# Performance work log

Measured on AMD Instinct MI355X. Metric: run time of the kernel, lower is better.

Reference implementation:

```python
import jax, jax.numpy as jnp
import numpy as np

B, S, D_IN, D, H, HD, HALF, L = 64, 500, 64, 128, 8, 16, 5, 2
WIN = 2 * HALF + 1  # 11 attended positions per query
EPS = 1e-12  # HF layer_norm_eps default


def _ln(x, g, b):
    m = x.mean(-1, keepdims=True)
    v = ((x - m) ** 2).mean(-1, keepdims=True)
    return (x - m) / jnp.sqrt(v + EPS) * g + b


def setup_inputs() -> dict:
    key = jax.random.key(0)
    ks = jax.random.split(key, 24)
    n = lambda i, shape: jax.random.normal(ks[i], shape, jnp.float32) * 0.02
    return {
        "x": jax.random.normal(ks[0], (B, S, D_IN), jnp.float32),
        "W_in": n(1, (D_IN, D)), "b_in": jnp.zeros((D,), jnp.float32),
        "pos_emb": n(2, (512, D)), "tt_emb": n(3, (D,)),
        "ln_emb_g": jnp.ones((D,), jnp.float32), "ln_emb_b": jnp.zeros((D,), jnp.float32),
        "Wq": n(4, (L, D, D)), "bq": jnp.zeros((L, D), jnp.float32),
        "Wk": n(5, (L, D, D)), "bk": jnp.zeros((L, D), jnp.float32),
        "Wv": n(6, (L, D, D)), "bv": jnp.zeros((L, D), jnp.float32),
        "Wo": n(7, (L, D, D)), "bo": jnp.zeros((L, D), jnp.float32),
        "ln1_g": jnp.ones((L, D), jnp.float32), "ln1_b": jnp.zeros((L, D), jnp.float32),
        "Wi": n(8, (L, D, 512)), "bi": jnp.zeros((L, 512), jnp.float32),
        "Wo2": n(9, (L, 512, D)), "bo2": jnp.zeros((L, D), jnp.float32),
        "ln2_g": jnp.ones((L, D), jnp.float32), "ln2_b": jnp.zeros((L, D), jnp.float32),
        "W_cls": n(10, (D, 2)), "b_cls": jnp.zeros((2,), jnp.float32),
    }


def reference(x, W_in, b_in, pos_emb, tt_emb, ln_emb_g, ln_emb_b,
              Wq, bq, Wk, bk, Wv, bv, Wo, bo, ln1_g, ln1_b,
              Wi, bi, Wo2, bo2, ln2_g, ln2_b, W_cls, b_cls):
    # input projection + RoBERTa-style embeddings (position ids start at padding_idx+1=2)
    h = x @ W_in + b_in
    pos_ids = 2 + jnp.arange(S)
    h = _ln(h + pos_emb[pos_ids] + tt_emb, ln_emb_g, ln_emb_b)

    # sliding-window gather indices: each query attends [i-HALF, i+HALF]
    idx = jnp.arange(S)[:, None] + jnp.arange(-HALF, HALF + 1)[None, :]
    valid = (idx >= 0) & (idx < S)
    idxc = jnp.clip(idx, 0, S - 1)
    scale = 1.0 / jnp.sqrt(jnp.float32(HD))

    for l in range(L):
        qh = (h @ Wq[l] + bq[l]).reshape(B, S, H, HD).transpose(0, 2, 1, 3)
        kh = (h @ Wk[l] + bk[l]).reshape(B, S, H, HD).transpose(0, 2, 1, 3)
        vh = (h @ Wv[l] + bv[l]).reshape(B, S, H, HD).transpose(0, 2, 1, 3)
        kk = kh[:, :, idxc]
        scores = jnp.einsum('bhsd,bhswd->bhsw', qh * scale, kk)
        scores = jnp.where(valid, scores, -jnp.inf)
        probs = jax.nn.softmax(scores, axis=-1)
        vv = vh[:, :, idxc]
        ctx = jnp.einsum('bhsw,bhswd->bhsd', probs, vv)
        ctx = ctx.transpose(0, 2, 1, 3).reshape(B, S, D)
        h = _ln(ctx @ Wo[l] + bo[l] + h, ln1_g[l], ln1_b[l])
        ff = jax.nn.gelu(h @ Wi[l] + bi[l], approximate=False) @ Wo2[l] + bo2[l]
        h = _ln(ff + h, ln2_g[l], ln2_b[l])

    pooled = h.mean(axis=1)  # mean over sequence
    return pooled @ W_cls + b_cls
```

## Files before the change

kernel.cpp:

```cpp
#include <hip/hip_runtime.h>
#include <hip/hip_bf16.h>
#include <math.h>

#define BB 64
#define SS 500
#define DIN 64
#define DD 128
#define HH 8
#define HDIM 16
#define HALF_ 5
#define WINW 11
#define LL 2
#define FF 512
#define MM (BB*SS)
#define LN_EPS 1e-12f

typedef __attribute__((ext_vector_type(8))) short short8;
typedef __attribute__((ext_vector_type(4))) float f32x4;

__global__ __launch_bounds__(256) void k_prep(
    const float* __restrict__ Wq, const float* __restrict__ Wk,
    const float* __restrict__ Wv, const float* __restrict__ Wo,
    const float* __restrict__ Wi, const float* __restrict__ Wo2,
    const float* __restrict__ Win, __hip_bfloat16* __restrict__ wT)
{
    const int m = blockIdx.y;
    const float* src; int Kd, Nd, kshift, doff;
    if (m == 12) {
        src = Win; Kd = 64; Nd = 128; kshift = 6; doff = 393216;
    } else {
        const int l = m / 6, t = m % 6;
        int toff;
        switch (t) {
          case 0:  src = Wq  + l*16384; Kd=128; Nd=128; kshift=7; toff=0;      break;
          case 1:  src = Wk  + l*16384; Kd=128; Nd=128; kshift=7; toff=16384;  break;
          case 2:  src = Wv  + l*16384; Kd=128; Nd=128; kshift=7; toff=32768;  break;
          case 3:  src = Wo  + l*16384; Kd=128; Nd=128; kshift=7; toff=49152;  break;
          case 4:  src = Wi  + l*65536; Kd=128; Nd=512; kshift=7; toff=65536;  break;
          default: src = Wo2 + l*65536; Kd=512; Nd=128; kshift=9; toff=131072; break;
        }
        doff = l*196608 + toff;
    }
    __hip_bfloat16* dst = wT + doff;
    const int NK = Kd * Nd;
    int e = (blockIdx.x * 256 + threadIdx.x) * 4;
    if (e >= NK) return;
    #pragma unroll
    for (int j = 0; j < 4; ++j, ++e) {
        int n = e >> kshift, kx = e & (Kd - 1);
        dst[(size_t)n * Kd + kx] = __float2bfloat16(src[(size_t)kx * Nd + n]);
    }
}

__global__ __launch_bounds__(256) void k_xcvt(
    const float* __restrict__ x, __hip_bfloat16* __restrict__ xbf)
{
    int i = (blockIdx.x * 256 + threadIdx.x) * 4;
    if (i >= MM * DIN) return;
    float4 v = *(const float4*)(x + i);
    ushort4 o;
    __hip_bfloat16 t0 = __float2bfloat16(v.x); o.x = *(unsigned short*)&t0;
    __hip_bfloat16 t1 = __float2bfloat16(v.y); o.y = *(unsigned short*)&t1;
    __hip_bfloat16 t2 = __float2bfloat16(v.z); o.z = *(unsigned short*)&t2;
    __hip_bfloat16 t3 = __float2bfloat16(v.w); o.w = *(unsigned short*)&t3;
    *(ushort4*)(xbf + i) = o;
}

#define GEMM_MAIN(Abf, lda, Kdim, WTbf, ldw, n0w)                             \
    __shared__ __align__(16) __hip_bfloat16 As[64][72];                       \
    __shared__ __align__(16) __hip_bfloat16 Ws[128][72];                      \
    const int tid = threadIdx.x;                                              \
    const int wid = tid >> 6;                                                 \
    const int l15 = tid & 15;                                                 \
    const int l4  = (tid & 63) >> 4;                                          \
    const int m0  = blockIdx.x * 64;                                          \
    f32x4 acc[8];                                                             \
    _Pragma("unroll")                                                         \
    for (int n = 0; n < 8; ++n) acc[n] = (f32x4){0.f, 0.f, 0.f, 0.f};         \
    for (int k0 = 0; k0 < (Kdim); k0 += 64) {                                 \
        _Pragma("unroll")                                                     \
        for (int it = 0; it < 2; ++it) {                                      \
            int lin = it * 2048 + tid * 8;                                    \
            int r = lin >> 6, c = lin & 63;                                   \
            *(uint4*)&As[r][c] =                                              \
                *(const uint4*)((Abf) + (size_t)(m0 + r) * (lda) + k0 + c);   \
        }                                                                     \
        _Pragma("unroll")                                                     \
        for (int it = 0; it < 4; ++it) {                                      \
            int lin = it * 2048 + tid * 8;                                    \
            int r = lin >> 6, c = lin & 63;                                   \
            *(uint4*)&Ws[r][c] =                                              \
                *(const uint4*)((WTbf) + (size_t)((n0w) + r) * (ldw) + k0 + c); \
        }                                                                     \
        __syncthreads();                                                      \
        _Pragma("unroll")                                                     \
        for (int kc = 0; kc < 64; kc += 32) {                                 \
            short8 a0 = *(const short8*)&As[wid * 16 + l15][kc + l4 * 8];     \
            _Pragma("unroll")                                                 \
            for (int n = 0; n < 8; ++n) {                                     \
                short8 bf = *(const short8*)&Ws[n * 16 + l15][kc + l4 * 8];   \
                acc[n] = __builtin_amdgcn_mfma_f32_16x16x32_bf16(a0, bf, acc[n], 0, 0, 0); \
            }                                                                 \
        }                                                                     \
        __syncthreads();                                                      \
    }

__global__ __launch_bounds__(256, 4) void k_embed(
    const __hip_bfloat16* __restrict__ xbf, const __hip_bfloat16* __restrict__ wInT,
    const float* __restrict__ bin, const float* __restrict__ pos,
    const float* __restrict__ tt, const float* __restrict__ g,
    const float* __restrict__ be, float* __restrict__ h,
    __hip_bfloat16* __restrict__ hbf)
{
    GEMM_MAIN(xbf, DIN, DIN, wInT, DIN, 0)
    #pragma unroll
    for (int qq = 0; qq < 4; ++qq) {
        const int row = m0 + wid * 16 + l4 * 4 + qq;
        const int s = row % SS;
        float vals[8]; float s1 = 0.f, s2 = 0.f;
        #pragma unroll
        for (int n = 0; n < 8; ++n) {
            const int col = n * 16 + l15;
            float val = acc[n][qq] + bin[col] + tt[col] + pos[(size_t)(2 + s) * DD + col];
            vals[n] = val; s1 += val; s2 += val * val;
        }
        #pragma unroll
        for (int o = 1; o < 16; o <<= 1) {
            s1 += __shfl_xor(s1, o, 16);
            s2 += __shfl_xor(s2, o, 16);
        }
        const float mean = s1 * (1.0f / DD);
        const float var  = s2 * (1.0f / DD) - mean * mean;
        const float rstd = rsqrtf(var + LN_EPS);
        #pragma unroll
        for (int n = 0; n < 8; ++n) {
            const int col = n * 16 + l15;
            const float o = (vals[n] - mean) * rstd * g[col] + be[col];
            h[(size_t)row * DD + col]   = o;
            hbf[(size_t)row * DD + col] = __float2bfloat16(o);
        }
    }
}

__global__ __launch_bounds__(512, 4) void k_fused(
    const __hip_bfloat16* __restrict__ hin,
    const __hip_bfloat16* __restrict__ wTq, const __hip_bfloat16* __restrict__ wTk,
    const __hip_bfloat16* __restrict__ wTv, const __hip_bfloat16* __restrict__ wTo,
    const float* __restrict__ bq, const float* __restrict__ bk,
    const float* __restrict__ bv, const float* __restrict__ bo,
    const float* __restrict__ hres,
    const float* __restrict__ g1, const float* __restrict__ bt1,
    float* __restrict__ hout, __hip_bfloat16* __restrict__ hbfout)
{
    __shared__ __align__(16) char smem[51072];
    __hip_bfloat16* kS   = (__hip_bfloat16*)smem;
    __hip_bfloat16* vS   = (__hip_bfloat16*)(smem + 13056);
    __hip_bfloat16* hS   = (__hip_bfloat16*)(smem + 26112);
    __hip_bfloat16* qS   = (__hip_bfloat16*)(smem + 39168);
    float*          pS   = (float*)(smem + 47872);
    float*          rsum = (float*)(smem + 50048);
    __hip_bfloat16* ctxS = hS;

    const int tid = threadIdx.x;
    const int wid = tid >> 6;
    const int l15 = tid & 15, l4 = (tid & 63) >> 4;
    const int b = blockIdx.y;
    const int s0 = blockIdx.x * 32;

    #pragma unroll
    for (int it = 0; it < 2; ++it) {
        int lin = it * 512 + tid;
        if (lin < 768) {
            int r = lin >> 4, c8 = (lin & 15) * 8;
            int s = s0 - 5 + r;
            uint4 val = {0, 0, 0, 0};
            if (s >= 0 && s < SS)
                val = *(const uint4*)(hin + ((size_t)(b * SS + s)) * DD + c8);
            *(uint4*)&hS[r * 136 + c8] = val;
        }
    }
    __syncthreads();

    #pragma unroll
    for (int i = 0; i < 9; ++i) {
        const int t = wid + i * 8;
        const int out = t / 24;
        const int rem = t - out * 24;
        const int rt = rem >> 3, n = rem & 7;
        const __hip_bfloat16* WT = (out == 0) ? wTq : ((out == 1) ? wTk : wTv);
        const float* bias = (out == 0) ? bq : ((out == 1) ? bk : bv);
        f32x4 a = (f32x4){0.f, 0.f, 0.f, 0.f};
        #pragma unroll
        for (int kc = 0; kc < 4; ++kc) {
            short8 af  = *(const short8*)&hS[(rt * 16 + l15) * 136 + kc * 32 + l4 * 8];
            short8 bfg = *(const short8*)(WT + (size_t)(n * 16 + l15) * DD + kc * 32 + l4 * 8);
            a = __builtin_amdgcn_mfma_f32_16x16x32_bf16(af, bfg, a, 0, 0, 0);
        }
        const int col = n * 16 + l15;
        const float bcol = bias[col];
        #pragma unroll
        for (int qq = 0; qq < 4; ++qq) {
            const int row = rt * 16 + l4 * 4 + qq;
            const float val = a[qq] + bcol;
            if (out == 0) {
                if (row >= 5 && row < 37)
                    qS[(row - 5) * 136 + col] = __float2bfloat16(val * 0.25f);
            } else if (out == 1) {
                kS[row * 136 + col] = __float2bfloat16(val);
            } else {
                vS[row * 136 + col] = __float2bfloat16(val);
            }
        }
    }
    __syncthreads();

    {
        const int g = tid >> 4, wl = tid & 15;
        const int sq = s0 + g;
        const int sk = sq + wl - HALF_;
        const bool valid = (wl < WINW) && (sq < SS) && (sk >= 0) && (sk < SS);
        #pragma unroll
        for (int hh = 0; hh < 8; ++hh) {
            const int off = hh * 16;
            float sc = 0.f;
            const unsigned* qp = (const unsigned*)&qS[g * 136 + off];
            const unsigned* kp = (const unsigned*)&kS[(g + wl) * 136 + off];
            #pragma unroll
            for (int d2 = 0; d2 < 8; ++d2) {
                unsigned qu = qp[d2], ku = kp[d2];
                sc += __uint_as_float(qu << 16) * __uint_as_float(ku << 16)
                    + __uint_as_float(qu & 0xffff0000u) * __uint_as_float(ku & 0xffff0000u);
            }
            sc = valid ? sc : -INFINITY;
            float mx = sc;
            #pragma unroll
            for (int o = 1; o < 16; o <<= 1) mx = fmaxf(mx, __shfl_xor(mx, o, 16));
            float p = valid ? __expf(sc - mx) : 0.f;
            float den = p;
            #pragma unroll
            for (int o = 1; o < 16; o <<= 1) den += __shfl_xor(den, o, 16);
            const float inv = (den > 0.f) ? 1.f / den : 0.f;
            pS[g * 17 + wl] = p;
            float cd = 0.f;
            #pragma unroll
            for (int w2 = 0; w2 < WINW; ++w2)
                cd += pS[g * 17 + w2] * __bfloat162float(vS[(g + w2) * 136 + off + wl]);
            ctxS[g * 136 + off + wl] = __float2bfloat16(cd * inv);
        }
    }
    __syncthreads();

    const int rt2 = wid & 1, nh = wid >> 1;
    f32x4 ac[2];
    #pragma unroll
    for (int n4 = 0; n4 < 2; ++n4) {
        ac[n4] = (f32x4){0.f, 0.f, 0.f, 0.f};
        const int n = nh * 2 + n4;
        #pragma unroll
        for (int kc = 0; kc < 4; ++kc) {
            short8 af  = *(const short8*)&ctxS[(rt2 * 16 + l15) * 136 + kc * 32 + l4 * 8];
            short8 bfg = *(const short8*)(wTo + (size_t)(n * 16 + l15) * DD + kc * 32 + l4 * 8);
            ac[n4] = __builtin_amdgcn_mfma_f32_16x16x32_bf16(af, bfg, ac[n4], 0, 0, 0);
        }
    }
    float vals[4][2];
    #pragma unroll
    for (int qq = 0; qq < 4; ++qq) {
        const int r16 = l4 * 4 + qq;
        const int qrow = rt2 * 16 + r16;
        const int sq = s0 + qrow;
        const bool vr = (sq < SS);
        float s1 = 0.f, s2 = 0.f;
        #pragma unroll
        for (int n4 = 0; n4 < 2; ++n4) {
            const int col = (nh * 2 + n4) * 16 + l15;
            const float resv = vr ? hres[((size_t)(b * SS + sq)) * DD + col] : 0.f;
            const float val = ac[n4][qq] + bo[col] + resv;
            vals[qq][n4] = val; s1 += val; s2 += val * val;
        }
        #pragma unroll
        for (int o = 1; o < 16; o <<= 1) {
            s1 += __shfl_xor(s1, o, 16);
            s2 += __shfl_xor(s2, o, 16);
        }
        if (l15 == 0) {
            rsum[((rt2 * 4 + nh) * 16 + r16) * 2]     = s1;
            rsum[((rt2 * 4 + nh) * 16 + r16) * 2 + 1] = s2;
        }
    }
    __syncthreads();
    #pragma unroll
    for (int qq = 0; qq < 4; ++qq) {
        const int r16 = l4 * 4 + qq;
        const int qrow = rt2 * 16 + r16;
        const int sq = s0 + qrow;
        if (sq >= SS) continue;
        float S1 = 0.f, S2 = 0.f;
        #pragma unroll
        for (int j = 0; j < 4; ++j) {
            S1 += rsum[((rt2 * 4 + j) * 16 + r16) * 2];
            S2 += rsum[((rt2 * 4 + j) * 16 + r16) * 2 + 1];
        }
        const float mean = S1 * (1.0f / DD);
        const float var  = S2 * (1.0f / DD) - mean * mean;
        const float rstd = rsqrtf(var + LN_EPS);
        #pragma unroll
        for (int n4 = 0; n4 < 2; ++n4) {
            const int col = (nh * 2 + n4) * 16 + l15;
            const float o = (vals[qq][n4] - mean) * rstd * g1[col] + bt1[col];
            hout[((size_t)(b * SS + sq)) * DD + col]   = o;
            hbfout[((size_t)(b * SS + sq)) * DD + col] = __float2bfloat16(o);
        }
    }
}

__global__ __launch_bounds__(256, 4) void k_gemm_gelu(
    const __hip_bfloat16* __restrict__ hbf,
    const __hip_bfloat16* __restrict__ wTi,
    const float* __restrict__ bias, __hip_bfloat16* __restrict__ hid)
{
    const int n0g = blockIdx.y * 128;
    GEMM_MAIN(hbf, DD, DD, wTi, DD, n0g)
    #pragma unroll
    for (int qq = 0; qq < 4; ++qq) {
        const int row = m0 + wid * 16 + l4 * 4 + qq;
        #pragma unroll
        for (int n = 0; n < 8; ++n) {
            const int col = n0g + n * 16 + l15;
            float val = acc[n][qq] + bias[col];
            val = 0.5f * val * (1.f + erff(val * 0.70710678118f));
            hid[(size_t)row * FF + col] = __float2bfloat16(val);
        }
    }
}

__global__ __launch_bounds__(256, 4) void k_gemm_lnres(
    const __hip_bfloat16* __restrict__ Abf, int lda, int Kdim,
    const __hip_bfloat16* __restrict__ WT,
    const float* __restrict__ bias, const float* __restrict__ res,
    const float* __restrict__ g, const float* __restrict__ bt,
    float* __restrict__ outF, __hip_bfloat16* __restrict__ outB)
{
    GEMM_MAIN(Abf, lda, Kdim, WT, Kdim, 0)
    #pragma unroll
    for (int qq = 0; qq < 4; ++qq) {
        const int row = m0 + wid * 16 + l4 * 4 + qq;
        float vals[8]; float s1 = 0.f, s2 = 0.f;
        #pragma unroll
        for (int n = 0; n < 8; ++n) {
            const int col = n * 16 + l15;
            float val = acc[n][qq] + bias[col] + res[(size_t)row * DD + col];
            vals[n] = val; s1 += val; s2 += val * val;
        }
        #pragma unroll
        for (int o = 1; o < 16; o <<= 1) {
            s1 += __shfl_xor(s1, o, 16);
            s2 += __shfl_xor(s2, o, 16);
        }
        const float mean = s1 * (1.0f / DD);
        const float var  = s2 * (1.0f / DD) - mean * mean;
        const float rstd = rsqrtf(var + LN_EPS);
        #pragma unroll
        for (int n = 0; n < 8; ++n) {
            const int col = n * 16 + l15;
            const float o = (vals[n] - mean) * rstd * g[col] + bt[col];
            outF[(size_t)row * DD + col] = o;
            outB[(size_t)row * DD + col] = __float2bfloat16(o);
        }
    }
}

__global__ __launch_bounds__(128) void k_final(
    const float* __restrict__ h, const float* __restrict__ Wc,
    const float* __restrict__ bc, float* __restrict__ out)
{
    const int b = blockIdx.x, d = threadIdx.x;
    float p = 0.f;
    for (int s = 0; s < SS; ++s) p += h[((size_t)(b * SS + s)) * DD + d];
    p *= (1.0f / SS);
    float l0 = p * Wc[d * 2 + 0];
    float l1 = p * Wc[d * 2 + 1];
    #pragma unroll
    for (int off = 1; off < 64; off <<= 1) {
        l0 += __shfl_xor(l0, off);
        l1 += __shfl_xor(l1, off);
    }
    __shared__ float r[2][2];
    const int wid = d >> 6;
    if ((d & 63) == 0) { r[wid][0] = l0; r[wid][1] = l1; }
    __syncthreads();
    if (d == 0) {
        out[b * 2 + 0] = r[0][0] + r[1][0] + bc[0];
        out[b * 2 + 1] = r[0][1] + r[1][1] + bc[1];
    }
}

extern "C" void kernel_launch(void* const* d_in, const int* in_sizes, int n_in,
                              void* d_out, int out_size, void* d_ws, size_t ws_size,
                              hipStream_t stream)
{
    const float* x      = (const float*)d_in[0];
    const float* W_in   = (const float*)d_in[1];
    const float* b_in   = (const float*)d_in[2];
    const float* pos    = (const float*)d_in[3];
    const float* tt     = (const float*)d_in[4];
    const float* lng    = (const float*)d_in[5];
    const float* lnb    = (const float*)d_in[6];
    const float* Wq     = (const float*)d_in[7];
    const float* bq     = (const float*)d_in[8];
    const float* Wk     = (const float*)d_in[9];
    const float* bk     = (const float*)d_in[10];
    const float* Wv     = (const float*)d_in[11];
    const float* bv     = (const float*)d_in[12];
    const float* Wo     = (const float*)d_in[13];
    const float* bo     = (const float*)d_in[14];
    const float* ln1g   = (const float*)d_in[15];
    const float* ln1b   = (const float*)d_in[16];
    const float* Wi     = (const float*)d_in[17];
    const float* bi     = (const float*)d_in[18];
    const float* Wo2    = (const float*)d_in[19];
    const float* bo2    = (const float*)d_in[20];
    const float* ln2g   = (const float*)d_in[21];
    const float* ln2b   = (const float*)d_in[22];
    const float* Wc     = (const float*)d_in[23];
    const float* bc     = (const float*)d_in[24];

    float*          ws   = (float*)d_ws;
    float*          hA   = ws;
    __hip_bfloat16* hbA  = (__hip_bfloat16*)(ws + 4096000);
    __hip_bfloat16* xbf  = (__hip_bfloat16*)(ws + 6144000);
    __hip_bfloat16* wT   = (__hip_bfloat16*)(ws + 7168000);
    __hip_bfloat16* hid  = (__hip_bfloat16*)(ws + 7368704);
    float*          hB   = ws + 15560704;
    __hip_bfloat16* hbB  = (__hip_bfloat16*)(ws + 19656704);

    k_prep<<<dim3(64, 13), 256, 0, stream>>>(Wq, Wk, Wv, Wo, Wi, Wo2, W_in, wT);
    k_xcvt<<<2000, 256, 0, stream>>>(x, xbf);
    k_embed<<<MM / 64, 256, 0, stream>>>(xbf, wT + 393216, b_in, pos, tt, lng, lnb,
                                         hA, hbA);

    float* hI = hA; __hip_bfloat16* hbI = hbA;
    float* hO = hB; __hip_bfloat16* hbO = hbB;
    for (int l = 0; l < LL; ++l) {
        const __hip_bfloat16* wTq  = wT + l * 196608;
        const __hip_bfloat16* wTk  = wTq + 16384;
        const __hip_bfloat16* wTv  = wTq + 32768;
        const __hip_bfloat16* wTo  = wTq + 49152;
        const __hip_bfloat16* wTi  = wTq + 65536;
        const __hip_bfloat16* wTo2 = wTq + 131072;

        k_fused<<<dim3(16, BB), 512, 0, stream>>>(
            hbI, wTq, wTk, wTv, wTo,
            bq + l * DD, bk + l * DD, bv + l * DD, bo + l * DD,
            hI, ln1g + l * DD, ln1b + l * DD, hO, hbO);

        k_gemm_gelu<<<dim3(MM / 64, 4), 256, 0, stream>>>(
            hbO, wTi, bi + l * FF, hid);

        k_gemm_lnres<<<dim3(MM / 64, 1), 256, 0, stream>>>(
            hid, FF, FF, wTo2, bo2 + l * DD, hO, ln2g + l * DD, ln2b + l * DD,
            hO, hbO);

        float* tf = hI; hI = hO; hO = tf;
        __hip_bfloat16* tb = hbI; hbI = hbO; hbO = tb;
    }

    k_final<<<BB, 128, 0, stream>>>(hI, Wc, bc, (float*)d_out);
}
```

Baseline: 336.8 us.

## Fuse FFN up-projection, GELU and down-projection into the attention kernel

Folds the FFN (Wi GEMM plus GELU, then the Wo2 GEMM with residual and LayerNorm) into the per-tile attention kernel. The post-LN1 activations and the 32x512 hidden tile stay in shared memory, reusing the K/V/h/q buffers. This removes two kernel launches per layer and the global write and read of the bf16 hidden tensor. In exchange, only 32 rows are processed per block, so FFN weight reuse is lower, and weights are read straight from global memory for every block.

```diff
diff --git a/kernel.cpp b/kernel.cpp
--- a/kernel.cpp
+++ b/kernel.cpp
@@ -146,10 +146,13 @@
     const __hip_bfloat16* __restrict__ hin,
     const __hip_bfloat16* __restrict__ wTq, const __hip_bfloat16* __restrict__ wTk,
     const __hip_bfloat16* __restrict__ wTv, const __hip_bfloat16* __restrict__ wTo,
+    const __hip_bfloat16* __restrict__ wTi, const __hip_bfloat16* __restrict__ wTo2,
     const float* __restrict__ bq, const float* __restrict__ bk,
     const float* __restrict__ bv, const float* __restrict__ bo,
+    const float* __restrict__ bi, const float* __restrict__ bo2,
     const float* __restrict__ hres,
     const float* __restrict__ g1, const float* __restrict__ bt1,
+    const float* __restrict__ g2, const float* __restrict__ bt2,
     float* __restrict__ hout, __hip_bfloat16* __restrict__ hbfout)
 {
     __shared__ __align__(16) char smem[51072];
@@ -160,6 +163,8 @@
     float*          pS   = (float*)(smem + 47872);
     float*          rsum = (float*)(smem + 50048);
     __hip_bfloat16* ctxS = hS;
+    __hip_bfloat16* h1S  = qS;
+    __hip_bfloat16* hidS = (__hip_bfloat16*)smem;
 
     const int tid = threadIdx.x;
     const int wid = tid >> 6;
@@ -251,121 +256,148 @@
     __syncthreads();
 
     const int rt2 = wid & 1, nh = wid >> 1;
-    f32x4 ac[2];
-    #pragma unroll
-    for (int n4 = 0; n4 < 2; ++n4) {
-        ac[n4] = (f32x4){0.f, 0.f, 0.f, 0.f};
-        const int n = nh * 2 + n4;
-        #pragma unroll
-        for (int kc = 0; kc < 4; ++kc) {
-            short8 af  = *(const short8*)&ctxS[(rt2 * 16 + l15) * 136 + kc * 32 + l4 * 8];
-            short8 bfg = *(const short8*)(wTo + (size_t)(n * 16 + l15) * DD + kc * 32 + l4 * 8);
-            ac[n4] = __builtin_amdgcn_mfma_f32_16x16x32_bf16(af, bfg, ac[n4], 0, 0, 0);
-        }
-    }
-    float vals[4][2];
-    #pragma unroll
-    for (int qq = 0; qq < 4; ++qq) {
-        const int r16 = l4 * 4 + qq;
-        const int qrow = rt2 * 16 + r16;
-        const int sq = s0 + qrow;
-        const bool vr = (sq < SS);
-        float s1 = 0.f, s2 = 0.f;
+    {
+        f32x4 ac[2];
         #pragma unroll
         for (int n4 = 0; n4 < 2; ++n4) {
-            const int col = (nh * 2 + n4) * 16 + l15;
-            const float resv = vr ? hres[((size_t)(b * SS + sq)) * DD + col] : 0.f;
-            const float val = ac[n4][qq] + bo[col] + resv;
-            vals[qq][n4] = val; s1 += val; s2 += val * val;
-        }
-        #pragma unroll
-        for (int o = 1; o < 16; o <<= 1) {
-            s1 += __shfl_xor(s1, o, 16);
-            s2 += __shfl_xor(s2, o, 16);
-        }
-        if (l15 == 0) {
-            rsum[((rt2 * 4 + nh) * 16 + r16) * 2]     = s1;
-            rsum[((rt2 * 4 + nh) * 16 + r16) * 2 + 1] = s2;
-        }
-    }
-    __syncthreads();
-    #pragma unroll
-    for (int qq = 0; qq < 4; ++qq) {
-        const int r16 = l4 * 4 + qq;
-        const int qrow = rt2 * 16 + r16;
-        const int sq = s0 + qrow;
-        if (sq >= SS) continue;
-        float S1 = 0.f, S2 = 0.f;
-        #pragma unroll
-        for (int j = 0; j < 4; ++j) {
-            S1 += rsum[((rt2 * 4 + j) * 16 + r16) * 2];
-            S2 += rsum[((rt2 * 4 + j) * 16 + r16) * 2 + 1];
-        }
-        const float mean = S1 * (1.0f / DD);
-        const float var  = S2 * (1.0f / DD) - mean * mean;
-        const float rstd = rsqrtf(var + LN_EPS);
+            ac[n4] = (f32x4){0.f, 0.f, 0.f, 0.f};
+            const int n = nh * 2 + n4;
+            #pragma unroll
+            for (int kc = 0; kc < 4; ++kc) {
+                short8 af  = *(const short8*)&ctxS[(rt2 * 16 + l15) * 136 + kc * 32 + l4 * 8];
+                short8 bfg = *(const short8*)(wTo + (size_t)(n * 16 + l15) * DD + kc * 32 + l4 * 8);
+                ac[n4] = __builtin_amdgcn_mfma_f32_16x16x32_bf16(af, bfg, ac[n4], 0, 0, 0);
+            }
+        }
+        float vals[4][2];
+        #pragma unroll
+        for (int qq = 0; qq < 4; ++qq) {
+            const int r16 = l4 * 4 + qq;
+            const int qrow = rt2 * 16 + r16;
+            const int sq = s0 + qrow;
+            const bool vr = (sq < SS);
+            float s1 = 0.f, s2 = 0.f;
+            #pragma unroll
+            for (int n4 = 0; n4 < 2; ++n4) {
+                const int col = (nh * 2 + n4) * 16 + l15;
+                const float resv = vr ? hres[((size_t)(b * SS + sq)) * DD + col] : 0.f;
+                const float val = ac[n4][qq] + bo[col] + resv;
+                vals[qq][n4] = val; s1 += val; s2 += val * val;
+            }
+            #pragma unroll
+            for (int o = 1; o < 16; o <<= 1) {
+                s1 += __shfl_xor(s1, o, 16);
+                s2 += __shfl_xor(s2, o, 16);
+            }
+            if (l15 == 0) {
+                rsum[((rt2 * 4 + nh) * 16 + r16) * 2]     = s1;
+                rsum[((rt2 * 4 + nh) * 16 + r16) * 2 + 1] = s2;
+            }
+        }
+        __syncthreads();
+        #pragma unroll
+        for (int qq = 0; qq < 4; ++qq) {
+            const int r16 = l4 * 4 + qq;
+            const int qrow = rt2 * 16 + r16;
+            float S1 = 0.f, S2 = 0.f;
+            #pragma unroll
+            for (int j = 0; j < 4; ++j) {
+                S1 += rsum[((rt2 * 4 + j) * 16 + r16) * 2];
+                S2 += rsum[((rt2 * 4 + j) * 16 + r16) * 2 + 1];
+            }
+            const float mean = S1 * (1.0f / DD);
+            const float var  = S2 * (1.0f / DD) - mean * mean;
+            const float rstd = rsqrtf(fmaxf(var, 0.f) + LN_EPS);
+            #pragma unroll
+            for (int n4 = 0; n4 < 2; ++n4) {
+                const int col = (nh * 2 + n4) * 16 + l15;
+                const float o = (vals[qq][n4] - mean) * rstd * g1[col] + bt1[col];
+                vals[qq][n4] = o;
+                h1S[qrow * 136 + col] = __float2bfloat16(o);
+            }
+        }
+        __syncthreads();
+
+        #pragma unroll
+        for (int i = 0; i < 8; ++i) {
+            const int t = wid + i * 8;
+            const int rt = t >> 5, n = t & 31;
+            f32x4 a = (f32x4){0.f, 0.f, 0.f, 0.f};
+            #pragma unroll
+            for (int kc = 0; kc < 4; ++kc) {
+                short8 af  = *(const short8*)&h1S[(rt * 16 + l15) * 136 + kc * 32 + l4 * 8];
+                short8 bfg = *(const short8*)(wTi + (size_t)(n * 16 + l15) * DD + kc * 32 + l4 * 8);
+                a = __builtin_amdgcn_mfma_f32_16x16x32_bf16(af, bfg, a, 0, 0, 0);
+            }
+            const int col = n * 16 + l15;
+            const float bcol = bi[col];
+            #pragma unroll
+            for (int qq = 0; qq < 4; ++qq) {
+                const int row = rt * 16 + l4 * 4 + qq;
+                float val = a[qq] + bcol;
+                val = 0.5f * val * (1.f + erff(val * 0.70710678118f));
+                hidS[row * 520 + col] = __float2bfloat16(val);
+            }
+        }
+        __syncthreads();
+
+        f32x4 a2[2];
         #pragma unroll
         for (int n4 = 0; n4 < 2; ++n4) {
-            const int col = (nh * 2 + n4) * 16 + l15;
-            const float o = (vals[qq][n4] - mean) * rstd * g1[col] + bt1[col];
-            hout[((size_t)(b * SS + sq)) * DD + col]   = o;
-            hbfout[((size_t)(b * SS + sq)) * DD + col] = __float2bfloat16(o);
-        }
-    }
-}
-
-__global__ __launch_bounds__(256, 4) void k_gemm_gelu(
-    const __hip_bfloat16* __restrict__ hbf,
-    const __hip_bfloat16* __restrict__ wTi,
-    const float* __restrict__ bias, __hip_bfloat16* __restrict__ hid)
-{
-    const int n0g = blockIdx.y * 128;
-    GEMM_MAIN(hbf, DD, DD, wTi, DD, n0g)
-    #pragma unroll
-    for (int qq = 0; qq < 4; ++qq) {
-        const int row = m0 + wid * 16 + l4 * 4 + qq;
-        #pragma unroll
-        for (int n = 0; n < 8; ++n) {
-            const int col = n0g + n * 16 + l15;
-            float val = acc[n][qq] + bias[col];
-            val = 0.5f * val * (1.f + erff(val * 0.70710678118f));
-            hid[(size_t)row * FF + col] = __float2bfloat16(val);
-        }
-    }
-}
-
-__global__ __launch_bounds__(256, 4) void k_gemm_lnres(
-    const __hip_bfloat16* __restrict__ Abf, int lda, int Kdim,
-    const __hip_bfloat16* __restrict__ WT,
-    const float* __restrict__ bias, const float* __restrict__ res,
-    const float* __restrict__ g, const float* __restrict__ bt,
-    float* __restrict__ outF, __hip_bfloat16* __restrict__ outB)
-{
-    GEMM_MAIN(Abf, lda, Kdim, WT, Kdim, 0)
-    #pragma unroll
-    for (int qq = 0; qq < 4; ++qq) {
-        const int row = m0 + wid * 16 + l4 * 4 + qq;
-        float vals[8]; float s1 = 0.f, s2 = 0.f;
-        #pragma unroll
-        for (int n = 0; n < 8; ++n) {
-            const int col = n * 16 + l15;
-            float val = acc[n][qq] + bias[col] + res[(size_t)row * DD + col];
-            vals[n] = val; s1 += val; s2 += val * val;
-        }
-        #pragma unroll
-        for (int o = 1; o < 16; o <<= 1) {
-            s1 += __shfl_xor(s1, o, 16);
-            s2 += __shfl_xor(s2, o, 16);
-        }
-        const float mean = s1 * (1.0f / DD);
-        const float var  = s2 * (1.0f / DD) - mean * mean;
-        const float rstd = rsqrtf(var + LN_EPS);
-        #pragma unroll
-        for (int n = 0; n < 8; ++n) {
-            const int col = n * 16 + l15;
-            const float o = (vals[n] - mean) * rstd * g[col] + bt[col];
-            outF[(size_t)row * DD + col] = o;
-            outB[(size_t)row * DD + col] = __float2bfloat16(o);
+            a2[n4] = (f32x4){0.f, 0.f, 0.f, 0.f};
+            const int n = nh * 2 + n4;
+            #pragma unroll
+            for (int ks = 0; ks < 16; ++ks) {
+                short8 af  = *(const short8*)&hidS[(rt2 * 16 + l15) * 520 + ks * 32 + l4 * 8];
+                short8 bfg = *(const short8*)(wTo2 + (size_t)(n * 16 + l15) * FF + ks * 32 + l4 * 8);
+                a2[n4] = __builtin_amdgcn_mfma_f32_16x16x32_bf16(af, bfg, a2[n4], 0, 0, 0);
+            }
+        }
+        float vals2[4][2];
+        __syncthreads();
+        #pragma unroll
+        for (int qq = 0; qq < 4; ++qq) {
+            const int r16 = l4 * 4 + qq;
+            float s1 = 0.f, s2 = 0.f;
+            #pragma unroll
+            for (int n4 = 0; n4 < 2; ++n4) {
+                const int col = (nh * 2 + n4) * 16 + l15;
+                const float val = a2[n4][qq] + bo2[col] + vals[qq][n4];
+                vals2[qq][n4] = val; s1 += val; s2 += val * val;
+            }
+            #pragma unroll
+            for (int o = 1; o < 16; o <<= 1) {
+                s1 += __shfl_xor(s1, o, 16);
+                s2 += __shfl_xor(s2, o, 16);
+            }
+            if (l15 == 0) {
+                rsum[((rt2 * 4 + nh) * 16 + r16) * 2]     = s1;
+                rsum[((rt2 * 4 + nh) * 16 + r16) * 2 + 1] = s2;
+            }
+        }
+        __syncthreads();
+        #pragma unroll
+        for (int qq = 0; qq < 4; ++qq) {
+            const int r16 = l4 * 4 + qq;
+            const int qrow = rt2 * 16 + r16;
+            const int sq = s0 + qrow;
+            if (sq >= SS) continue;
+            float S1 = 0.f, S2 = 0.f;
+            #pragma unroll
+            for (int j = 0; j < 4; ++j) {
+                S1 += rsum[((rt2 * 4 + j) * 16 + r16) * 2];
+                S2 += rsum[((rt2 * 4 + j) * 16 + r16) * 2 + 1];
+            }
+            const float mean = S1 * (1.0f / DD);
+            const float var  = S2 * (1.0f / DD) - mean * mean;
+            const float rstd = rsqrtf(fmaxf(var, 0.f) + LN_EPS);
+            #pragma unroll
+            for (int n4 = 0; n4 < 2; ++n4) {
+                const int col = (nh * 2 + n4) * 16 + l15;
+                const float o = (vals2[qq][n4] - mean) * rstd * g2[col] + bt2[col];
+                hout[((size_t)(b * SS + sq)) * DD + col]   = o;
+                hbfout[((size_t)(b * SS + sq)) * DD + col] = __float2bfloat16(o);
+            }
         }
     }
 }
@@ -430,9 +462,8 @@
     __hip_bfloat16* hbA  = (__hip_bfloat16*)(ws + 4096000);
     __hip_bfloat16* xbf  = (__hip_bfloat16*)(ws + 6144000);
     __hip_bfloat16* wT   = (__hip_bfloat16*)(ws + 7168000);
-    __hip_bfloat16* hid  = (__hip_bfloat16*)(ws + 7368704);
-    float*          hB   = ws + 15560704;
-    __hip_bfloat16* hbB  = (__hip_bfloat16*)(ws + 19656704);
+    float*          hB   = ws + 7368704;
+    __hip_bfloat16* hbB  = (__hip_bfloat16*)(ws + 11464704);
 
     k_prep<<<dim3(64, 13), 256, 0, stream>>>(Wq, Wk, Wv, Wo, Wi, Wo2, W_in, wT);
     k_xcvt<<<2000, 256, 0, stream>>>(x, xbf);
@@ -450,15 +481,10 @@
         const __hip_bfloat16* wTo2 = wTq + 131072;
 
         k_fused<<<dim3(16, BB), 512, 0, stream>>>(
-            hbI, wTq, wTk, wTv, wTo,
+            hbI, wTq, wTk, wTv, wTo, wTi, wTo2,
             bq + l * DD, bk + l * DD, bv + l * DD, bo + l * DD,
-            hI, ln1g + l * DD, ln1b + l * DD, hO, hbO);
-
-        k_gemm_gelu<<<dim3(MM / 64, 4), 256, 0, stream>>>(
-            hbO, wTi, bi + l * FF, hid);
-
-        k_gemm_lnres<<<dim3(MM / 64, 1), 256, 0, stream>>>(
-            hid, FF, FF, wTo2, bo2 + l * DD, hO, ln2g + l * DD, ln2b + l * DD,
+            bi + l * FF, bo2 + l * DD,
+            hI, ln1g + l * DD, ln1b + l * DD, ln2g + l * DD, ln2b + l * DD,
             hO, hbO);
 
         float* tf = hI; hI = hO; hO = tf;
```

New measurement: 346.2 us. 2.8% more time.
